# Optimization experiments

Hardware: AMD Instinct MI355X
Metric: run time of the kernel (lower is better)

The kernel has to match this reference:

```python
import jax, jax.numpy as jnp
import numpy as np


def log_g(x):
    # log(relu(x) + 0.5) for x >= 0, else -softplus(-x)
    pos = jnp.log(jnp.maximum(x, 0.0) + 0.5)
    neg = -jax.nn.softplus(-x)
    return jnp.where(x >= 0, pos, neg)


def parallel_scan_log(log_coeffs, log_values):
    # h_t = a_t * h_{t-1} + b_t, computed stably in log space
    a_star = jnp.cumsum(log_coeffs, axis=1)
    log_h0_plus_b_star = jax.lax.cumlogsumexp(log_values - a_star, axis=1)
    log_h = a_star + log_h0_plus_b_star
    return jnp.exp(log_h)


def setup_inputs() -> dict:
    key = jax.random.key(0)
    k1, k2 = jax.random.split(key)
    B, S, D = 8, 4096, 1024
    x = jax.random.normal(k1, (B, S, D), dtype=jnp.float32)
    # torch nn.Linear(dim, 2*inner_dim, bias=False): weight [2*inner_dim, dim]
    W_hg = jax.random.normal(k2, (2 * D, D), dtype=jnp.float32) * (1.0 / np.sqrt(D))
    return {"x": x, "W_hg": W_hg}


def reference(x, W_hg):
    # hidden_gate projection: [B,S,D] @ [D, 2*inner] -> [B,S,2*inner]
    hg = jnp.einsum("bsd,ed->bse", x, W_hg)
    hidden, gate = jnp.split(hg, 2, axis=-1)
    log_coeffs = -jax.nn.softplus(gate)       # log(1 - z)
    log_z = -jax.nn.softplus(-gate)           # log(z)
    log_tilde_h = log_g(hidden)
    log_values = log_z + log_tilde_h
    out = parallel_scan_log(log_coeffs, log_values)
    # expansion_factor == 1.0 -> self.out is Identity; dropout_prob == 0 -> Identity
    return out
```

## Files before the change

### kernel.cpp

```cpp
#include <hip/hip_runtime.h>

#define B_   8
#define S_   4096
#define D_   1024
#define M_   (B_ * S_)
#define N_   (2 * D_)
#define K_   D_
#define CCH  128
#define LCH  32

#define BK   32
#define NT   (K_ / BK)

typedef __attribute__((ext_vector_type(8))) short bf16x8;
typedef __attribute__((ext_vector_type(4))) float f32x4;

__device__ __forceinline__ unsigned short f2bf(float f) {
  union { float f; unsigned u; } v; v.f = f;
  unsigned u = v.u;
  u = u + 0x7fffu + ((u >> 16) & 1u);
  return (unsigned short)(u >> 16);
}
__device__ __forceinline__ float bf2f(unsigned short h) {
  union { unsigned u; float f; } v; v.u = ((unsigned)h) << 16;
  return v.f;
}
__device__ __forceinline__ float sigmoidf_(float x) {
  return 1.0f / (1.0f + __expf(-x));
}

#define GLL(src, dst) __builtin_amdgcn_global_load_lds(                     \
      (const __attribute__((address_space(1))) void*)(src),                 \
      (__attribute__((address_space(3))) void*)(dst), 16, 0, 0)

__global__ __launch_bounds__(256) void k_cvt2(const float* __restrict__ x,
                                              const float* __restrict__ W,
                                              unsigned short* __restrict__ xb,
                                              unsigned short* __restrict__ wb) {
  const int n4x = (M_ * K_) / 4;
  const int n4t = n4x + (N_ * K_) / 4;
  int i = blockIdx.x * 256 + threadIdx.x;
  const int stride = gridDim.x * 256;
  for (; i < n4t; i += stride) {
    const float4* src = (i < n4x) ? &reinterpret_cast<const float4*>(x)[i]
                                  : &reinterpret_cast<const float4*>(W)[i - n4x];
    float4 v = *src;
    ushort4 o;
    o.x = f2bf(v.x); o.y = f2bf(v.y); o.z = f2bf(v.z); o.w = f2bf(v.w);
    if (i < n4x) reinterpret_cast<ushort4*>(xb)[i] = o;
    else         reinterpret_cast<ushort4*>(wb)[i - n4x] = o;
  }
}

__global__ __launch_bounds__(512, 4) void k_gemm(const unsigned short* __restrict__ xb,
                                                 const unsigned short* __restrict__ wb,
                                                 unsigned short* __restrict__ Gp,
                                                 unsigned short* __restrict__ Zp) {
  __shared__ unsigned short lds[36864];
  const int tid = threadIdx.x;
  int wg = blockIdx.x;
  wg = (wg & 7) * 256 + (wg >> 3);
  const int bm = wg >> 4;
  const int bn = wg & 15;
  const int lane = tid & 63;
  const int wid = tid >> 6;
  const int wrr = wid >> 1;
  const int wcc = wid & 1;
  const int fr = lane & 15;
  const int hi = lane >> 4;

  const int srow = tid >> 2;
  const int scol = ((tid & 3) ^ ((srow >> 1) & 3)) * 16;
  const char* aS = (const char*)xb + (size_t)(bm * 256 + srow) * 2048 + scol;
  const char* bS = (const char*)wb + (size_t)(bn * 128 + srow) * 2048 + scol;
  char* const ldsc = (char*)lds + (size_t)tid * 16;
  const char* const ldsr = (const char*)lds;

  const int sA = ((hi ^ ((fr >> 1) & 3)) * 16);
  const int arow = (wrr * 64 + fr) * 64;
  const int brow = 16384 + (wcc * 64 + fr) * 64;

  f32x4 acc[4][4] = {};
  bf16x8 av[4], bv[4];

  GLL(aS,               ldsc);
  GLL(aS + 262144,      ldsc + 8192);
  GLL(bS,               ldsc + 16384);
  GLL(aS + 64,          ldsc + 24576);
  GLL(aS + 262144 + 64, ldsc + 32768);
  GLL(bS + 64,          ldsc + 40960);
  asm volatile("s_waitcnt vmcnt(3)\n\ts_barrier" ::: "memory");

  int sl = 0;
  int sn = 49152;

  for (int t = 0; t < NT; ++t) {
    const bool st2 = (t < NT - 2);
    if (st2) {
      const size_t kb = (size_t)(t + 2) * 64;
      char* dq = ldsc + sn;
      GLL(aS + kb,               dq);
      GLL(aS + 262144 + kb,      dq + 8192);
      GLL(bS + kb,               dq + 16384);
    }
    const char* Ab = ldsr + sl;
#pragma unroll
    for (int m = 0; m < 4; ++m)
      av[m] = *(const bf16x8*)(Ab + arow + m * 1024 + sA);
#pragma unroll
    for (int n = 0; n < 4; ++n)
      bv[n] = *(const bf16x8*)(Ab + brow + n * 1024 + sA);
    __builtin_amdgcn_s_setprio(1);
#pragma unroll
    for (int m = 0; m < 4; ++m)
#pragma unroll
      for (int n = 0; n < 4; ++n)
        acc[m][n] = __builtin_amdgcn_mfma_f32_16x16x32_bf16(av[m], bv[n], acc[m][n], 0, 0, 0);
    __builtin_amdgcn_s_setprio(0);
    if (st2) asm volatile("s_waitcnt vmcnt(3)\n\ts_barrier" ::: "memory");
    else     asm volatile("s_waitcnt vmcnt(0)\n\ts_barrier" ::: "memory");
    sl += 24576; if (sl == 73728) sl = 0;
    sn += 24576; if (sn == 73728) sn = 0;
  }

  const int row0 = bm * 256 + wrr * 64 + (hi << 2);
  const int col0 = bn * 128 + wcc * 64 + fr;
  if (bn < 8) {
#pragma unroll
    for (int m = 0; m < 4; ++m)
#pragma unroll
      for (int n = 0; n < 4; ++n)
#pragma unroll
        for (int i = 0; i < 4; ++i) {
          float v = acc[m][n][i];
          float g = (v >= 0.0f) ? (v + 0.5f) : sigmoidf_(v);
          Gp[(size_t)(row0 + m * 16 + i) * 1024 + (col0 + n * 16)] = f2bf(g);
        }
  } else {
#pragma unroll
    for (int m = 0; m < 4; ++m)
#pragma unroll
      for (int n = 0; n < 4; ++n)
#pragma unroll
        for (int i = 0; i < 4; ++i) {
          float v = acc[m][n][i];
          Zp[(size_t)(row0 + m * 16 + i) * 1024 + (col0 + n * 16 - 1024)] = f2bf(sigmoidf_(v));
        }
  }
}

__global__ __launch_bounds__(256) void k_scan1(const unsigned short* __restrict__ Gp,
                                               const unsigned short* __restrict__ Zp,
                                               float* __restrict__ Ap,
                                               float* __restrict__ Hp) {
  const int gid = blockIdx.x * 256 + threadIdx.x;
  const int c = blockIdx.y;
  const int b = gid >> 8;
  const int d0 = (gid & 255) << 2;
  size_t base = ((size_t)b * S_ + (size_t)c * LCH) * 1024 + d0;
  float4 aP = {1.f, 1.f, 1.f, 1.f};
  float4 h  = {0.f, 0.f, 0.f, 0.f};
#pragma unroll 8
  for (int s = 0; s < LCH; ++s) {
    ushort4 zu = *reinterpret_cast<const ushort4*>(Zp + base);
    ushort4 gu = *reinterpret_cast<const ushort4*>(Gp + base);
    float z0 = bf2f(zu.x), z1 = bf2f(zu.y), z2 = bf2f(zu.z), z3 = bf2f(zu.w);
    float a0 = 1.f - z0,   a1 = 1.f - z1,   a2 = 1.f - z2,   a3 = 1.f - z3;
    h.x = fmaf(a0, h.x, z0 * bf2f(gu.x));
    h.y = fmaf(a1, h.y, z1 * bf2f(gu.y));
    h.z = fmaf(a2, h.z, z2 * bf2f(gu.z));
    h.w = fmaf(a3, h.w, z3 * bf2f(gu.w));
    aP.x *= a0; aP.y *= a1; aP.z *= a2; aP.w *= a3;
    base += 1024;
  }
  reinterpret_cast<float4*>(Ap)[(size_t)c * 2048 + gid] = aP;
  reinterpret_cast<float4*>(Hp)[(size_t)c * 2048 + gid] = h;
}

__global__ __launch_bounds__(256) void k_scan2(const float* __restrict__ Ap,
                                               const float* __restrict__ Hp,
                                               float* __restrict__ Cin) {
  const int gid = blockIdx.x * 256 + threadIdx.x;
  float4 carry = {0.f, 0.f, 0.f, 0.f};
  for (int c = 0; c < CCH; ++c) {
    reinterpret_cast<float4*>(Cin)[(size_t)c * 2048 + gid] = carry;
    float4 a = reinterpret_cast<const float4*>(Ap)[(size_t)c * 2048 + gid];
    float4 hh = reinterpret_cast<const float4*>(Hp)[(size_t)c * 2048 + gid];
    carry.x = fmaf(a.x, carry.x, hh.x);
    carry.y = fmaf(a.y, carry.y, hh.y);
    carry.z = fmaf(a.z, carry.z, hh.z);
    carry.w = fmaf(a.w, carry.w, hh.w);
  }
}

__global__ __launch_bounds__(256) void k_scan3(const unsigned short* __restrict__ Gp,
                                               const unsigned short* __restrict__ Zp,
                                               const float* __restrict__ Cin,
                                               float* __restrict__ out) {
  const int gid = blockIdx.x * 256 + threadIdx.x;
  const int c = blockIdx.y;
  const int b = gid >> 8;
  const int d0 = (gid & 255) << 2;
  size_t base = ((size_t)b * S_ + (size_t)c * LCH) * 1024 + d0;
  float4 h = reinterpret_cast<const float4*>(Cin)[(size_t)c * 2048 + gid];
#pragma unroll 8
  for (int s = 0; s < LCH; ++s) {
    ushort4 zu = *reinterpret_cast<const ushort4*>(Zp + base);
    ushort4 gu = *reinterpret_cast<const ushort4*>(Gp + base);
    float z0 = bf2f(zu.x), z1 = bf2f(zu.y), z2 = bf2f(zu.z), z3 = bf2f(zu.w);
    h.x = fmaf(1.f - z0, h.x, z0 * bf2f(gu.x));
    h.y = fmaf(1.f - z1, h.y, z1 * bf2f(gu.y));
    h.z = fmaf(1.f - z2, h.z, z2 * bf2f(gu.z));
    h.w = fmaf(1.f - z3, h.w, z3 * bf2f(gu.w));
    *reinterpret_cast<float4*>(out + base) = h;
    base += 1024;
  }
}

extern "C" void kernel_launch(void* const* d_in, const int* in_sizes, int n_in,
                              void* d_out, int out_size, void* d_ws, size_t ws_size,
                              hipStream_t stream) {
  const float* x = (const float*)d_in[0];
  const float* W = (const float*)d_in[1];
  float* out = (float*)d_out;

  unsigned char* w = (unsigned char*)d_ws;
  unsigned short* xb = (unsigned short*)(w);
  unsigned short* wb = (unsigned short*)(w + 67108864);
  unsigned short* Gp = (unsigned short*)(w + 67108864 + 4194304);
  unsigned short* Zp = (unsigned short*)(w + 67108864 + 4194304 + 67108864);
  float* Ap  = (float*)(w);
  float* Hp  = (float*)(w + 4194304);
  float* Cin = (float*)(w + 8388608);

  k_cvt2<<<4096, 256, 0, stream>>>(x, W, xb, wb);
  k_gemm<<<(M_ / 256) * (N_ / 128), 512, 0, stream>>>(xb, wb, Gp, Zp);
  k_scan1<<<dim3(8, CCH), 256, 0, stream>>>(Gp, Zp, Ap, Hp);
  k_scan2<<<8, 256, 0, stream>>>(Ap, Hp, Cin);
  k_scan3<<<dim3(8, CCH), 256, 0, stream>>>(Gp, Zp, Cin, out);
}
```

Baseline: 273.6 us.

## Fuse local chunk scan into GEMM epilogue, interleaving hidden/gate columns per tile

The GEMM tile now loads matching hidden and gate weight rows together, so each block has both halves for the same output columns. Its epilogue computes the gate coefficients and runs a 32-step local scan with wave shuffles, then writes the local prefix h and cumulative product a as bf16. The standalone first scan pass is dropped, the carry pass reads and updates the chunk-end values in place, and the final pass applies the carry with one FMA per element. This removes a full read of both intermediate tensors, at the cost of a heavier epilogue and bf16 rounding of the cumulative products and carries.

```diff
diff --git a/kernel.cpp b/kernel.cpp
--- a/kernel.cpp
+++ b/kernel.cpp
@@ -54,8 +54,8 @@
 
 __global__ __launch_bounds__(512, 4) void k_gemm(const unsigned short* __restrict__ xb,
                                                  const unsigned short* __restrict__ wb,
-                                                 unsigned short* __restrict__ Gp,
-                                                 unsigned short* __restrict__ Zp) {
+                                                 unsigned short* __restrict__ HLp,
+                                                 unsigned short* __restrict__ APp) {
   __shared__ unsigned short lds[36864];
   const int tid = threadIdx.x;
   int wg = blockIdx.x;
@@ -72,16 +72,19 @@
   const int srow = tid >> 2;
   const int scol = ((tid & 3) ^ ((srow >> 1) & 3)) * 16;
   const char* aS = (const char*)xb + (size_t)(bm * 256 + srow) * 2048 + scol;
-  const char* bS = (const char*)wb + (size_t)(bn * 128 + srow) * 2048 + scol;
+  const char* bS = (const char*)wb +
+      (size_t)(bn * 64 + srow + ((srow >= 64) ? 960 : 0)) * 2048 + scol;
   char* const ldsc = (char*)lds + (size_t)tid * 16;
   const char* const ldsr = (const char*)lds;
 
   const int sA = ((hi ^ ((fr >> 1) & 3)) * 16);
-  const int arow = (wrr * 64 + fr) * 64;
-  const int brow = 16384 + (wcc * 64 + fr) * 64;
-
-  f32x4 acc[4][4] = {};
-  bf16x8 av[4], bv[4];
+  const int arow  = (wrr * 64 + fr) * 64;
+  const int browH = 16384 + (wcc * 32 + fr) * 64;
+  const int browG = browH + 4096;
+
+  f32x4 accH[4][2] = {};
+  f32x4 accG[4][2] = {};
+  bf16x8 av[4], bvH[2], bvG[2];
 
   GLL(aS,               ldsc);
   GLL(aS + 262144,      ldsc + 8192);
@@ -99,23 +102,28 @@
     if (st2) {
       const size_t kb = (size_t)(t + 2) * 64;
       char* dq = ldsc + sn;
-      GLL(aS + kb,               dq);
-      GLL(aS + 262144 + kb,      dq + 8192);
-      GLL(bS + kb,               dq + 16384);
+      GLL(aS + kb,          dq);
+      GLL(aS + 262144 + kb, dq + 8192);
+      GLL(bS + kb,          dq + 16384);
     }
     const char* Ab = ldsr + sl;
 #pragma unroll
     for (int m = 0; m < 4; ++m)
       av[m] = *(const bf16x8*)(Ab + arow + m * 1024 + sA);
 #pragma unroll
-    for (int n = 0; n < 4; ++n)
-      bv[n] = *(const bf16x8*)(Ab + brow + n * 1024 + sA);
+    for (int n = 0; n < 2; ++n) {
+      bvH[n] = *(const bf16x8*)(Ab + browH + n * 1024 + sA);
+      bvG[n] = *(const bf16x8*)(Ab + browG + n * 1024 + sA);
+    }
     __builtin_amdgcn_s_setprio(1);
 #pragma unroll
-    for (int m = 0; m < 4; ++m)
-#pragma unroll
-      for (int n = 0; n < 4; ++n)
-        acc[m][n] = __builtin_amdgcn_mfma_f32_16x16x32_bf16(av[m], bv[n], acc[m][n], 0, 0, 0);
+    for (int m = 0; m < 4; ++m) {
+#pragma unroll
+      for (int n = 0; n < 2; ++n) {
+        accH[m][n] = __builtin_amdgcn_mfma_f32_16x16x32_bf16(av[m], bvH[n], accH[m][n], 0, 0, 0);
+        accG[m][n] = __builtin_amdgcn_mfma_f32_16x16x32_bf16(av[m], bvG[n], accG[m][n], 0, 0, 0);
+      }
+    }
     __builtin_amdgcn_s_setprio(0);
     if (st2) asm volatile("s_waitcnt vmcnt(3)\n\ts_barrier" ::: "memory");
     else     asm volatile("s_waitcnt vmcnt(0)\n\ts_barrier" ::: "memory");
@@ -123,98 +131,116 @@
     sn += 24576; if (sn == 73728) sn = 0;
   }
 
-  const int row0 = bm * 256 + wrr * 64 + (hi << 2);
-  const int col0 = bn * 128 + wcc * 64 + fr;
-  if (bn < 8) {
-#pragma unroll
-    for (int m = 0; m < 4; ++m)
-#pragma unroll
-      for (int n = 0; n < 4; ++n)
+  const int dcol0 = bn * 64 + wcc * 32 + fr;
+  const size_t rowg0 = (size_t)(bm * 256 + wrr * 64);
+#pragma unroll
+  for (int kap = 0; kap < 2; ++kap) {
+#pragma unroll
+    for (int n = 0; n < 2; ++n) {
+      float a_[2][4], b_[2][4];
+#pragma unroll
+      for (int mm = 0; mm < 2; ++mm)
 #pragma unroll
         for (int i = 0; i < 4; ++i) {
-          float v = acc[m][n][i];
-          float g = (v >= 0.0f) ? (v + 0.5f) : sigmoidf_(v);
-          Gp[(size_t)(row0 + m * 16 + i) * 1024 + (col0 + n * 16)] = f2bf(g);
+          float zg = sigmoidf_(accG[kap * 2 + mm][n][i]);
+          float hv = accH[kap * 2 + mm][n][i];
+          float gg = (hv >= 0.f) ? (hv + 0.5f) : sigmoidf_(hv);
+          a_[mm][i] = 1.f - zg;
+          b_[mm][i] = zg * gg;
         }
-  } else {
-#pragma unroll
-    for (int m = 0; m < 4; ++m)
-#pragma unroll
-      for (int n = 0; n < 4; ++n)
-#pragma unroll
-        for (int i = 0; i < 4; ++i) {
-          float v = acc[m][n][i];
-          Zp[(size_t)(row0 + m * 16 + i) * 1024 + (col0 + n * 16 - 1024)] = f2bf(sigmoidf_(v));
-        }
-  }
-}
-
-__global__ __launch_bounds__(256) void k_scan1(const unsigned short* __restrict__ Gp,
-                                               const unsigned short* __restrict__ Zp,
-                                               float* __restrict__ Ap,
-                                               float* __restrict__ Hp) {
+      float A1 = a_[0][0] * a_[0][1] * a_[0][2] * a_[0][3];
+      float B1 = ((b_[0][0] * a_[0][1] + b_[0][1]) * a_[0][2] + b_[0][2]) * a_[0][3] + b_[0][3];
+      float A2 = a_[1][0] * a_[1][1] * a_[1][2] * a_[1][3];
+      float B2 = ((b_[1][0] * a_[1][1] + b_[1][1]) * a_[1][2] + b_[1][2]) * a_[1][3] + b_[1][3];
+      float Ai = A1, Bi = B1;
+      { float Ao = __shfl(Ai, (lane - 16) & 63), Bo = __shfl(Bi, (lane - 16) & 63);
+        if (hi >= 1) { Bi += Ai * Bo; Ai *= Ao; } }
+      { float Ao = __shfl(Ai, (lane - 32) & 63), Bo = __shfl(Bi, (lane - 32) & 63);
+        if (hi >= 2) { Bi += Ai * Bo; Ai *= Ao; } }
+      float Ae1 = __shfl(Ai, (lane - 16) & 63), Be1 = __shfl(Bi, (lane - 16) & 63);
+      if (hi == 0) { Ae1 = 1.f; Be1 = 0.f; }
+      float At = __shfl(Ai, fr + 48), Bt = __shfl(Bi, fr + 48);
+      float Ai2 = A2, Bi2 = B2;
+      { float Ao = __shfl(Ai2, (lane - 16) & 63), Bo = __shfl(Bi2, (lane - 16) & 63);
+        if (hi >= 1) { Bi2 += Ai2 * Bo; Ai2 *= Ao; } }
+      { float Ao = __shfl(Ai2, (lane - 32) & 63), Bo = __shfl(Bi2, (lane - 32) & 63);
+        if (hi >= 2) { Bi2 += Ai2 * Bo; Ai2 *= Ao; } }
+      float Ae2 = __shfl(Ai2, (lane - 16) & 63), Be2 = __shfl(Bi2, (lane - 16) & 63);
+      if (hi == 0) { Ae2 = 1.f; Be2 = 0.f; }
+      const float Ax2 = Ae2 * At;
+      const float Bx2 = Be2 + Ae2 * Bt;
+      const int d = dcol0 + n * 16;
+      size_t rr = (rowg0 + kap * 32 + hi * 4) * 1024 + d;
+      float ap = Ae1, hl = Be1;
+#pragma unroll
+      for (int i = 0; i < 4; ++i) {
+        hl = a_[0][i] * hl + b_[0][i]; ap *= a_[0][i];
+        __builtin_nontemporal_store(f2bf(hl), &HLp[rr]);
+        __builtin_nontemporal_store(f2bf(ap), &APp[rr]);
+        rr += 1024;
+      }
+      rr = (rowg0 + kap * 32 + 16 + hi * 4) * 1024 + d;
+      ap = Ax2; hl = Bx2;
+#pragma unroll
+      for (int i = 0; i < 4; ++i) {
+        hl = a_[1][i] * hl + b_[1][i]; ap *= a_[1][i];
+        __builtin_nontemporal_store(f2bf(hl), &HLp[rr]);
+        __builtin_nontemporal_store(f2bf(ap), &APp[rr]);
+        rr += 1024;
+      }
+    }
+  }
+}
+
+__global__ __launch_bounds__(256) void k_scan2(unsigned short* __restrict__ HL,
+                                               const unsigned short* __restrict__ AP) {
   const int gid = blockIdx.x * 256 + threadIdx.x;
-  const int c = blockIdx.y;
   const int b = gid >> 8;
   const int d0 = (gid & 255) << 2;
-  size_t base = ((size_t)b * S_ + (size_t)c * LCH) * 1024 + d0;
-  float4 aP = {1.f, 1.f, 1.f, 1.f};
-  float4 h  = {0.f, 0.f, 0.f, 0.f};
-#pragma unroll 8
-  for (int s = 0; s < LCH; ++s) {
-    ushort4 zu = *reinterpret_cast<const ushort4*>(Zp + base);
-    ushort4 gu = *reinterpret_cast<const ushort4*>(Gp + base);
-    float z0 = bf2f(zu.x), z1 = bf2f(zu.y), z2 = bf2f(zu.z), z3 = bf2f(zu.w);
-    float a0 = 1.f - z0,   a1 = 1.f - z1,   a2 = 1.f - z2,   a3 = 1.f - z3;
-    h.x = fmaf(a0, h.x, z0 * bf2f(gu.x));
-    h.y = fmaf(a1, h.y, z1 * bf2f(gu.y));
-    h.z = fmaf(a2, h.z, z2 * bf2f(gu.z));
-    h.w = fmaf(a3, h.w, z3 * bf2f(gu.w));
-    aP.x *= a0; aP.y *= a1; aP.z *= a2; aP.w *= a3;
-    base += 1024;
-  }
-  reinterpret_cast<float4*>(Ap)[(size_t)c * 2048 + gid] = aP;
-  reinterpret_cast<float4*>(Hp)[(size_t)c * 2048 + gid] = h;
-}
-
-__global__ __launch_bounds__(256) void k_scan2(const float* __restrict__ Ap,
-                                               const float* __restrict__ Hp,
-                                               float* __restrict__ Cin) {
-  const int gid = blockIdx.x * 256 + threadIdx.x;
-  float4 carry = {0.f, 0.f, 0.f, 0.f};
+  float c0 = 0.f, c1 = 0.f, c2 = 0.f, c3 = 0.f;
   for (int c = 0; c < CCH; ++c) {
-    reinterpret_cast<float4*>(Cin)[(size_t)c * 2048 + gid] = carry;
-    float4 a = reinterpret_cast<const float4*>(Ap)[(size_t)c * 2048 + gid];
-    float4 hh = reinterpret_cast<const float4*>(Hp)[(size_t)c * 2048 + gid];
-    carry.x = fmaf(a.x, carry.x, hh.x);
-    carry.y = fmaf(a.y, carry.y, hh.y);
-    carry.z = fmaf(a.z, carry.z, hh.z);
-    carry.w = fmaf(a.w, carry.w, hh.w);
-  }
-}
-
-__global__ __launch_bounds__(256) void k_scan3(const unsigned short* __restrict__ Gp,
-                                               const unsigned short* __restrict__ Zp,
-                                               const float* __restrict__ Cin,
+    size_t off = ((size_t)b * S_ + (size_t)c * LCH + 31) * 1024 + d0;
+    ushort4 hu = *reinterpret_cast<const ushort4*>(HL + off);
+    ushort4 au = *reinterpret_cast<const ushort4*>(AP + off);
+    c0 = fmaf(bf2f(au.x), c0, bf2f(hu.x));
+    c1 = fmaf(bf2f(au.y), c1, bf2f(hu.y));
+    c2 = fmaf(bf2f(au.z), c2, bf2f(hu.z));
+    c3 = fmaf(bf2f(au.w), c3, bf2f(hu.w));
+    ushort4 o; o.x = f2bf(c0); o.y = f2bf(c1); o.z = f2bf(c2); o.w = f2bf(c3);
+    *reinterpret_cast<ushort4*>(HL + off) = o;
+  }
+}
+
+__global__ __launch_bounds__(256) void k_scan3(const unsigned short* __restrict__ HL,
+                                               const unsigned short* __restrict__ AP,
                                                float* __restrict__ out) {
   const int gid = blockIdx.x * 256 + threadIdx.x;
   const int c = blockIdx.y;
   const int b = gid >> 8;
   const int d0 = (gid & 255) << 2;
-  size_t base = ((size_t)b * S_ + (size_t)c * LCH) * 1024 + d0;
-  float4 h = reinterpret_cast<const float4*>(Cin)[(size_t)c * 2048 + gid];
+  const size_t rbase = (size_t)b * S_ + (size_t)c * LCH;
+  float4 carry = {0.f, 0.f, 0.f, 0.f};
+  if (c > 0) {
+    ushort4 cu = *reinterpret_cast<const ushort4*>(HL + (rbase - 1) * 1024 + d0);
+    carry.x = bf2f(cu.x); carry.y = bf2f(cu.y); carry.z = bf2f(cu.z); carry.w = bf2f(cu.w);
+  }
+  size_t off = rbase * 1024 + d0;
 #pragma unroll 8
-  for (int s = 0; s < LCH; ++s) {
-    ushort4 zu = *reinterpret_cast<const ushort4*>(Zp + base);
-    ushort4 gu = *reinterpret_cast<const ushort4*>(Gp + base);
-    float z0 = bf2f(zu.x), z1 = bf2f(zu.y), z2 = bf2f(zu.z), z3 = bf2f(zu.w);
-    h.x = fmaf(1.f - z0, h.x, z0 * bf2f(gu.x));
-    h.y = fmaf(1.f - z1, h.y, z1 * bf2f(gu.y));
-    h.z = fmaf(1.f - z2, h.z, z2 * bf2f(gu.z));
-    h.w = fmaf(1.f - z3, h.w, z3 * bf2f(gu.w));
-    *reinterpret_cast<float4*>(out + base) = h;
-    base += 1024;
-  }
+  for (int s = 0; s < LCH - 1; ++s) {
+    ushort4 hu = *reinterpret_cast<const ushort4*>(HL + off);
+    ushort4 au = *reinterpret_cast<const ushort4*>(AP + off);
+    float4 o;
+    o.x = fmaf(bf2f(au.x), carry.x, bf2f(hu.x));
+    o.y = fmaf(bf2f(au.y), carry.y, bf2f(hu.y));
+    o.z = fmaf(bf2f(au.z), carry.z, bf2f(hu.z));
+    o.w = fmaf(bf2f(au.w), carry.w, bf2f(hu.w));
+    *reinterpret_cast<float4*>(out + off) = o;
+    off += 1024;
+  }
+  ushort4 hu = *reinterpret_cast<const ushort4*>(HL + off);
+  float4 o;
+  o.x = bf2f(hu.x); o.y = bf2f(hu.y); o.z = bf2f(hu.z); o.w = bf2f(hu.w);
+  *reinterpret_cast<float4*>(out + off) = o;
 }
 
 extern "C" void kernel_launch(void* const* d_in, const int* in_sizes, int n_in,
@@ -225,17 +251,13 @@
   float* out = (float*)d_out;
 
   unsigned char* w = (unsigned char*)d_ws;
-  unsigned short* xb = (unsigned short*)(w);
-  unsigned short* wb = (unsigned short*)(w + 67108864);
-  unsigned short* Gp = (unsigned short*)(w + 67108864 + 4194304);
-  unsigned short* Zp = (unsigned short*)(w + 67108864 + 4194304 + 67108864);
-  float* Ap  = (float*)(w);
-  float* Hp  = (float*)(w + 4194304);
-  float* Cin = (float*)(w + 8388608);
+  unsigned short* xb  = (unsigned short*)(w);
+  unsigned short* wb  = (unsigned short*)(w + 67108864);
+  unsigned short* HLp = (unsigned short*)(w + 71303168);
+  unsigned short* APp = (unsigned short*)(w + 138412032);
 
   k_cvt2<<<4096, 256, 0, stream>>>(x, W, xb, wb);
-  k_gemm<<<(M_ / 256) * (N_ / 128), 512, 0, stream>>>(xb, wb, Gp, Zp);
-  k_scan1<<<dim3(8, CCH), 256, 0, stream>>>(Gp, Zp, Ap, Hp);
-  k_scan2<<<8, 256, 0, stream>>>(Ap, Hp, Cin);
-  k_scan3<<<dim3(8, CCH), 256, 0, stream>>>(Gp, Zp, Cin, out);
-}
+  k_gemm<<<(M_ / 256) * 16, 512, 0, stream>>>(xb, wb, HLp, APp);
+  k_scan2<<<8, 256, 0, stream>>>(HLp, APp);
+  k_scan3<<<dim3(8, CCH), 256, 0, stream>>>(HLp, APp, out);
+}
```

Result: slower. 362.5 us (+32.5%).
